# Kernel tuning notes

Hardware: AMD Instinct MI355X
Metric: run time of the kernel (lower is better)

Reference implementation:

```python
import jax, jax.numpy as jnp
import numpy as np

HEIGHT = 32
SIGMA = 2.0
NUM_NEGATIVE = 4096
N, C = 32, 512
L = HEIGHT * HEIGHT


def _grid_weight(height: int, sigma: float) -> jnp.ndarray:
    # distance_weights: pairwise Euclidean distance between grid points
    ii, jj = np.meshgrid(np.arange(height), np.arange(height), indexing='ij')
    coords = np.stack([ii.ravel(), jj.ravel()], axis=1).astype(np.float32)  # [L, 2]
    d2 = ((coords[:, None, :] - coords[None, :, :]) ** 2).sum(-1)  # squared dist [L, L]
    w = -(0.5 / sigma ** 2) * d2
    np.fill_diagonal(w, -np.inf)
    return jax.nn.softmax(jnp.asarray(w, dtype=jnp.float32), axis=1)


def setup_inputs() -> dict:
    key = jax.random.key(0)
    k1, k2 = jax.random.split(key)
    embedding = jax.random.normal(k1, (N, L, C), dtype=jnp.float32)
    weight = _grid_weight(HEIGHT, SIGMA)  # [L, L] softmax-normalized grid kernel
    neg_indices = jax.random.randint(k2, (NUM_NEGATIVE,), 0, N * L, dtype=jnp.int64)
    return {"embedding": embedding, "weight": weight, "neg_indices": neg_indices}


def reference(embedding, weight, neg_indices):
    n, l, c = embedding.shape
    # F.normalize(dim=-1), eps=1e-12
    norm = jnp.maximum(jnp.linalg.norm(embedding, axis=-1, keepdims=True), 1e-12)
    e = embedding / norm  # [N, L, C]
    # target = weight @ e  (broadcast over batch)
    target = jnp.einsum('kl,nlc->nkc', weight, e)  # [N, L, C]
    sim_pos = jnp.sum(e * target, axis=-1)  # [N, L]
    flat = e.reshape(-1, c)  # [N*L, C]
    negatives = flat[neg_indices]  # [M, C]
    sim_neg = jnp.einsum('nlc,mc->nlm', e, negatives)  # [N, L, M]
    logits = jnp.concatenate([sim_pos[..., None], sim_neg], axis=2).reshape(n * l, 1 + neg_indices.shape[0])
    # CrossEntropyLoss with target class 0, mean reduction
    loss = -jnp.mean(jax.nn.log_softmax(logits, axis=-1)[:, 0])
    return loss
```

## Files before the change

kernel.cpp:

```cpp
#include <hip/hip_runtime.h>
#include <hip/hip_bf16.h>
#include <stdint.h>

#define L_DIM 1024
#define C_DIM 512
#define CB4 256
#define N_BATCH 32
#define M_NEG 4096
#define NROWS (N_BATCH * L_DIM)

typedef float f32x4 __attribute__((ext_vector_type(4)));
typedef int i32x4 __attribute__((ext_vector_type(4)));
typedef int i32x8 __attribute__((ext_vector_type(8)));

#define E4_SCALE 32.0f
#define MX_SCALE 122
#define FMT_FP4 4

template <int GOFF>
__device__ __forceinline__ void gl_lds16(const uint8_t* g, uint8_t* l) {
  __builtin_amdgcn_global_load_lds(
      (const __attribute__((address_space(1))) void*)g,
      (__attribute__((address_space(3))) void*)l, 16, GOFF, 0);
}

__device__ __forceinline__ uint32_t fp4_enc(float x) {
  const uint32_t s = (__float_as_uint(x) >> 31) << 3;
  const float a = fabsf(x);
  uint32_t c;
  c = a < 0.25f ? 0u
    : a < 0.75f ? 1u
    : a < 1.25f ? 2u
    : a < 1.75f ? 3u
    : a < 2.5f  ? 4u
    : a < 3.5f  ? 5u
    : a < 5.0f  ? 6u : 7u;
  return s | c;
}

__device__ __forceinline__ i32x8 fp4_op(i32x4 d) {
  return __builtin_shufflevector(d, d, 0, 1, 2, 3, -1, -1, -1, -1);
}

__device__ __forceinline__ int swz(int row) { return (row >> 1) & 3; }

__global__ __launch_bounds__(256) void k_normalize(const float* __restrict__ emb,
                                                   uint8_t* __restrict__ out,
                                                   float* __restrict__ zerobuf,
                                                   float* __restrict__ loss_out) {
  if (blockIdx.x < 256) zerobuf[blockIdx.x * 256 + threadIdx.x] = 0.0f;
  if (blockIdx.x == 0 && threadIdx.x == 0) loss_out[0] = 0.0f;
  const int lane = threadIdx.x & 63;
  const int wave = threadIdx.x >> 6;
  const long row = (long)blockIdx.x * 4 + wave;
  const float4* src = (const float4*)(emb + row * C_DIM);
  float4 v0 = src[2 * lane];
  float4 v1 = src[2 * lane + 1];
  float ss = v0.x * v0.x + v0.y * v0.y + v0.z * v0.z + v0.w * v0.w +
             v1.x * v1.x + v1.y * v1.y + v1.z * v1.z + v1.w * v1.w;
#pragma unroll
  for (int off = 1; off < 64; off <<= 1) ss += __shfl_xor(ss, off, 64);
  const float s = E4_SCALE / fmaxf(sqrtf(ss), 1e-12f);
  uint32_t pk = fp4_enc(v0.x * s)        | (fp4_enc(v0.y * s) << 4) |
                (fp4_enc(v0.z * s) << 8) | (fp4_enc(v0.w * s) << 12) |
                (fp4_enc(v1.x * s) << 16)| (fp4_enc(v1.y * s) << 20) |
                (fp4_enc(v1.z * s) << 24)| (fp4_enc(v1.w * s) << 28);
  ((uint32_t*)(out + row * CB4))[lane] = pk;
}

__global__ __launch_bounds__(256, 4) void k_gemm_fused(
    const uint8_t* __restrict__ E4, const int* __restrict__ idx,
    const float* __restrict__ W, float* __restrict__ rowsum,
    float* __restrict__ simpos) {
  __shared__ __align__(16) unsigned char smem_raw[20480];
  uint8_t* sA = (uint8_t*)smem_raw;
  uint8_t* sB = sA + 128 * 64;

  const int tid = threadIdx.x;
  const int lane = tid & 63;
  const int wave = tid >> 6;
  const int wm = wave >> 1, wn = wave & 1;
  const int q = lane >> 4, c16 = lane & 15;

  const int bid = blockIdx.x;
  const bool is0 = bid >= 2048;
  long rowBase, colBase, n = 0;
  if (is0) {
    const int t = bid - 2048;
    const int xcd = t & 7, slot = t >> 3;
    rowBase = (long)(xcd * 32 + (slot & 31)) * 128;
    colBase = (long)(slot >> 5) * 128;
  } else {
    const int xcd = bid & 7, slot = bid >> 3;
    n = xcd * 4 + (slot & 3);
    const int inner = slot >> 2;
    rowBase = (long)(inner & 7) * 128;
    colBase = (long)(inner >> 3) * 128;
  }
  const long aBase = is0 ? rowBase : n * L_DIM + rowBase;

  const uint8_t* pA[2];
  const uint8_t* pB[2];
#pragma unroll
  for (int r = 0; r < 2; ++r) {
    const int c = r * 256 + tid;
    const int rw = c >> 2, cb = c & 3;
    pA[r] = E4 + (aBase + rw) * CB4 + (cb ^ swz(rw)) * 16;
    const long bRow = is0 ? (long)idx[colBase + rw] : n * L_DIM + colBase + rw;
    pB[r] = E4 + bRow * CB4 + (cb ^ swz(rw)) * 16;
  }

  int ldsB[4], ldsA[4];
#pragma unroll
  for (int j = 0; j < 4; ++j) {
    const int rowB = wn * 64 + j * 16 + c16;
    ldsB[j] = rowB * 64 + (q ^ swz(rowB)) * 16;
    const int rowA = wm * 64 + j * 16 + c16;
    ldsA[j] = rowA * 64 + (q ^ swz(rowA)) * 16;
  }

  f32x4 acc[4][4] = {};

  auto kstep = [&]() {
    __syncthreads();
    i32x8 bfr[4];
#pragma unroll
    for (int j = 0; j < 4; ++j)
      bfr[j] = fp4_op(*(const i32x4*)(sB + ldsB[j]));
#pragma unroll
    for (int i = 0; i < 4; ++i) {
      i32x8 af = fp4_op(*(const i32x4*)(sA + ldsA[i]));
#pragma unroll
      for (int j = 0; j < 4; ++j)
        acc[i][j] = __builtin_amdgcn_mfma_scale_f32_16x16x128_f8f6f4(
            af, bfr[j], acc[i][j], FMT_FP4, FMT_FP4,
            0, MX_SCALE, 0, MX_SCALE);
    }
    __syncthreads();
  };

  gl_lds16<0>(pA[0], sA + tid * 16);
  gl_lds16<0>(pA[1], sA + (256 + tid) * 16);
  gl_lds16<0>(pB[0], sB + tid * 16);
  gl_lds16<0>(pB[1], sB + (256 + tid) * 16);
  kstep();
  gl_lds16<64>(pA[0], sA + tid * 16);
  gl_lds16<64>(pA[1], sA + (256 + tid) * 16);
  gl_lds16<64>(pB[0], sB + tid * 16);
  gl_lds16<64>(pB[1], sB + (256 + tid) * 16);
  kstep();
  gl_lds16<128>(pA[0], sA + tid * 16);
  gl_lds16<128>(pA[1], sA + (256 + tid) * 16);
  gl_lds16<128>(pB[0], sB + tid * 16);
  gl_lds16<128>(pB[1], sB + (256 + tid) * 16);
  kstep();
  gl_lds16<192>(pA[0], sA + tid * 16);
  gl_lds16<192>(pA[1], sA + (256 + tid) * 16);
  gl_lds16<192>(pB[0], sB + tid * 16);
  gl_lds16<192>(pB[1], sB + (256 + tid) * 16);
  kstep();

  if (is0) {
    float* S = (float*)smem_raw;
#pragma unroll
    for (int i = 0; i < 4; ++i)
#pragma unroll
      for (int r = 0; r < 4; ++r) {
        const float s = __expf(acc[i][0][r]) + __expf(acc[i][1][r]) +
                        __expf(acc[i][2][r]) + __expf(acc[i][3][r]);
        S[wave * 1280 + (i * 16 + q * 4 + r) * 20 + c16] = s;
      }
    __syncthreads();
    if (tid < 128) {
      const int wm2 = tid >> 6, row64 = tid & 63;
      const float* p0 = (const float*)S + (wm2 * 2 + 0) * 1280 + row64 * 20;
      const float* p1 = (const float*)S + (wm2 * 2 + 1) * 1280 + row64 * 20;
      float4 t0 = ((const float4*)p0)[0], t1 = ((const float4*)p0)[1];
      float4 t2 = ((const float4*)p0)[2], t3 = ((const float4*)p0)[3];
      float4 u0 = ((const float4*)p1)[0], u1 = ((const float4*)p1)[1];
      float4 u2 = ((const float4*)p1)[2], u3 = ((const float4*)p1)[3];
      float v = t0.x + t0.y + t0.z + t0.w + t1.x + t1.y + t1.z + t1.w +
                t2.x + t2.y + t2.z + t2.w + t3.x + t3.y + t3.z + t3.w +
                u0.x + u0.y + u0.z + u0.w + u1.x + u1.y + u1.z + u1.w +
                u2.x + u2.y + u2.z + u2.w + u3.x + u3.y + u3.z + u3.w;
      atomicAdd(&rowsum[rowBase + tid], v);
    }
  } else {
    float* G = (float*)smem_raw;
#pragma unroll
    for (int p = 0; p < 4; ++p) {
      if (wm == (p >> 1)) {
#pragma unroll
        for (int ii = 0; ii < 2; ++ii) {
          const int i = (p & 1) * 2 + ii;
#pragma unroll
          for (int j = 0; j < 4; ++j)
#pragma unroll
            for (int r = 0; r < 4; ++r)
              G[(ii * 16 + q * 4 + r) * 132 + wn * 64 + j * 16 + c16] =
                  acc[i][j][r];
        }
      }
      __syncthreads();
      {
        const int rr = tid >> 3;
        const int chunk = tid & 7;
        const long krow = rowBase + p * 32 + rr;
        float v = 0.0f;
#pragma unroll
        for (int u = 0; u < 4; ++u) {
          const float4 g =
              *(const float4*)(G + rr * 132 + chunk * 16 + u * 4);
          const float4 w4 = *(const float4*)(W + krow * L_DIM + colBase +
                                             chunk * 16 + u * 4);
          v += g.x * w4.x + g.y * w4.y + g.z * w4.z + g.w * w4.w;
        }
        v += __shfl_xor(v, 1, 64);
        v += __shfl_xor(v, 2, 64);
        v += __shfl_xor(v, 4, 64);
        if (chunk == 0) atomicAdd(&simpos[n * L_DIM + krow], v);
      }
      __syncthreads();
    }
  }
}

__global__ __launch_bounds__(256) void k_finalize(const float* __restrict__ rowsum,
                                                  const float* __restrict__ simpos,
                                                  float* __restrict__ out) {
  const int gid = blockIdx.x * 256 + threadIdx.x;
  const float sp = simpos[gid];
  float v = __logf(rowsum[gid] + __expf(sp)) - sp;
#pragma unroll
  for (int off = 1; off < 64; off <<= 1) v += __shfl_xor(v, off, 64);
  __shared__ float ws[4];
  if ((threadIdx.x & 63) == 0) ws[threadIdx.x >> 6] = v;
  __syncthreads();
  if (threadIdx.x == 0)
    atomicAdd(out, (ws[0] + ws[1] + ws[2] + ws[3]) * (1.0f / (float)NROWS));
}

extern "C" void kernel_launch(void* const* d_in, const int* in_sizes, int n_in,
                              void* d_out, int out_size, void* d_ws, size_t ws_size,
                              hipStream_t stream) {
  const float* emb = (const float*)d_in[0];
  const float* weight = (const float*)d_in[1];
  const int* negidx = (const int*)d_in[2];
  float* out = (float*)d_out;
  char* ws = (char*)d_ws;

  uint8_t* E4 = (uint8_t*)ws;
  float* rowsum = (float*)(ws + 8388608);
  float* simpos = (float*)(ws + 8519680);

  k_normalize<<<NROWS / 4, 256, 0, stream>>>(emb, E4, rowsum, out);
  k_gemm_fused<<<10240, 256, 0, stream>>>(E4, negidx, weight, rowsum, simpos);
  k_finalize<<<NROWS / 256, 256, 0, stream>>>(rowsum, simpos, out);
}
```

Baseline: 165.0 us.

## Keep negative tile resident in LDS and stream embedding tiles per block

The negative-similarity GEMM blocks now load a 128-row negative tile (all K) into LDS once and loop over 8 embedding tiles of 128 rows. They accumulate exp sums per embedding row through shuffles and atomics rather than an LDS reduction. This cuts the grid from 10240 to 3072 blocks and removes repeated gathers of negative rows. The cost is doubled LDS (40KB) per block, which lowers occupancy, and less parallelism per block, with the exp-sum work serialized across the 8 tiles.

```diff
diff --git a/kernel.cpp b/kernel.cpp
--- a/kernel.cpp
+++ b/kernel.cpp
@@ -72,9 +72,7 @@
     const uint8_t* __restrict__ E4, const int* __restrict__ idx,
     const float* __restrict__ W, float* __restrict__ rowsum,
     float* __restrict__ simpos) {
-  __shared__ __align__(16) unsigned char smem_raw[20480];
-  uint8_t* sA = (uint8_t*)smem_raw;
-  uint8_t* sB = sA + 128 * 64;
+  __shared__ __align__(16) unsigned char smem_raw[40960];
 
   const int tid = threadIdx.x;
   const int lane = tid & 63;
@@ -83,109 +81,162 @@
   const int q = lane >> 4, c16 = lane & 15;
 
   const int bid = blockIdx.x;
-  const bool is0 = bid >= 2048;
-  long rowBase, colBase, n = 0;
-  if (is0) {
-    const int t = bid - 2048;
+
+  if (bid < 1024) {
+    uint8_t* sN = (uint8_t*)smem_raw;
+    uint8_t* sE = sN + 32768;
+    const int xcd = bid & 7, slot = bid >> 3;
+    const long negBase = (long)(slot & 31) * 128;
+    const long eBase0 = (long)(xcd * 4 + (slot >> 5)) * 1024;
+
+    const uint8_t* pN[2];
+#pragma unroll
+    for (int r = 0; r < 2; ++r) {
+      const int c = r * 256 + tid;
+      const int rw = c >> 2, cb = c & 3;
+      pN[r] = E4 + (long)idx[negBase + rw] * CB4 + (cb ^ swz(rw)) * 16;
+    }
+    gl_lds16<0>(pN[0], sN + tid * 16);
+    gl_lds16<0>(pN[1], sN + (256 + tid) * 16);
+    gl_lds16<64>(pN[0], sN + 8192 + tid * 16);
+    gl_lds16<64>(pN[1], sN + 8192 + (256 + tid) * 16);
+    gl_lds16<128>(pN[0], sN + 16384 + tid * 16);
+    gl_lds16<128>(pN[1], sN + 16384 + (256 + tid) * 16);
+    gl_lds16<192>(pN[0], sN + 24576 + tid * 16);
+    gl_lds16<192>(pN[1], sN + 24576 + (256 + tid) * 16);
+
+    const uint8_t* pE[2];
+#pragma unroll
+    for (int r = 0; r < 2; ++r) {
+      const int c = r * 256 + tid;
+      const int rw = c >> 2, cb = c & 3;
+      pE[r] = E4 + (eBase0 + rw) * CB4 + (cb ^ swz(rw)) * 16;
+    }
+
+    int ldsN[4], ldsE[4];
+#pragma unroll
+    for (int j = 0; j < 4; ++j) {
+      const int rowN = wm * 64 + j * 16 + c16;
+      ldsN[j] = rowN * 64 + (q ^ swz(rowN)) * 16;
+      const int rowE = wn * 64 + j * 16 + c16;
+      ldsE[j] = rowE * 64 + (q ^ swz(rowE)) * 16;
+    }
+
+    for (int et = 0; et < 8; ++et) {
+      f32x4 acc[4][4] = {};
+      auto kstep = [&](int ks) {
+        __syncthreads();
+        i32x8 efr[4];
+#pragma unroll
+        for (int j = 0; j < 4; ++j)
+          efr[j] = fp4_op(*(const i32x4*)(sE + ldsE[j]));
+#pragma unroll
+        for (int i = 0; i < 4; ++i) {
+          i32x8 nf = fp4_op(*(const i32x4*)(sN + ks * 8192 + ldsN[i]));
+#pragma unroll
+          for (int j = 0; j < 4; ++j)
+            acc[i][j] = __builtin_amdgcn_mfma_scale_f32_16x16x128_f8f6f4(
+                nf, efr[j], acc[i][j], FMT_FP4, FMT_FP4,
+                0, MX_SCALE, 0, MX_SCALE);
+        }
+        __syncthreads();
+      };
+      gl_lds16<0>(pE[0], sE + tid * 16);
+      gl_lds16<0>(pE[1], sE + (256 + tid) * 16);
+      kstep(0);
+      gl_lds16<64>(pE[0], sE + tid * 16);
+      gl_lds16<64>(pE[1], sE + (256 + tid) * 16);
+      kstep(1);
+      gl_lds16<128>(pE[0], sE + tid * 16);
+      gl_lds16<128>(pE[1], sE + (256 + tid) * 16);
+      kstep(2);
+      gl_lds16<192>(pE[0], sE + tid * 16);
+      gl_lds16<192>(pE[1], sE + (256 + tid) * 16);
+      kstep(3);
+      pE[0] += 32768;
+      pE[1] += 32768;
+
+      const long eCol = eBase0 + (long)et * 128 + wn * 64 + c16;
+#pragma unroll
+      for (int j = 0; j < 4; ++j) {
+        float s = 0.0f;
+#pragma unroll
+        for (int i = 0; i < 4; ++i)
+#pragma unroll
+          for (int r = 0; r < 4; ++r) s += __expf(acc[i][j][r]);
+        s += __shfl_xor(s, 16, 64);
+        s += __shfl_xor(s, 32, 64);
+        if (q == 0) atomicAdd(&rowsum[eCol + j * 16], s);
+      }
+    }
+  } else {
+    uint8_t* sA = (uint8_t*)smem_raw;
+    uint8_t* sB = sA + 8192;
+    const int t = bid - 1024;
     const int xcd = t & 7, slot = t >> 3;
-    rowBase = (long)(xcd * 32 + (slot & 31)) * 128;
-    colBase = (long)(slot >> 5) * 128;
-  } else {
-    const int xcd = bid & 7, slot = bid >> 3;
-    n = xcd * 4 + (slot & 3);
+    const long n = xcd * 4 + (slot & 3);
     const int inner = slot >> 2;
-    rowBase = (long)(inner & 7) * 128;
-    colBase = (long)(inner >> 3) * 128;
-  }
-  const long aBase = is0 ? rowBase : n * L_DIM + rowBase;
-
-  const uint8_t* pA[2];
-  const uint8_t* pB[2];
-#pragma unroll
-  for (int r = 0; r < 2; ++r) {
-    const int c = r * 256 + tid;
-    const int rw = c >> 2, cb = c & 3;
-    pA[r] = E4 + (aBase + rw) * CB4 + (cb ^ swz(rw)) * 16;
-    const long bRow = is0 ? (long)idx[colBase + rw] : n * L_DIM + colBase + rw;
-    pB[r] = E4 + bRow * CB4 + (cb ^ swz(rw)) * 16;
-  }
-
-  int ldsB[4], ldsA[4];
-#pragma unroll
-  for (int j = 0; j < 4; ++j) {
-    const int rowB = wn * 64 + j * 16 + c16;
-    ldsB[j] = rowB * 64 + (q ^ swz(rowB)) * 16;
-    const int rowA = wm * 64 + j * 16 + c16;
-    ldsA[j] = rowA * 64 + (q ^ swz(rowA)) * 16;
-  }
-
-  f32x4 acc[4][4] = {};
-
-  auto kstep = [&]() {
-    __syncthreads();
-    i32x8 bfr[4];
-#pragma unroll
-    for (int j = 0; j < 4; ++j)
-      bfr[j] = fp4_op(*(const i32x4*)(sB + ldsB[j]));
-#pragma unroll
-    for (int i = 0; i < 4; ++i) {
-      i32x8 af = fp4_op(*(const i32x4*)(sA + ldsA[i]));
+    const long rowBase = (long)(inner & 7) * 128;
+    const long colBase = (long)(inner >> 3) * 128;
+    const long aBase = n * L_DIM + rowBase;
+
+    const uint8_t* pA[2];
+    const uint8_t* pB[2];
+#pragma unroll
+    for (int r = 0; r < 2; ++r) {
+      const int c = r * 256 + tid;
+      const int rw = c >> 2, cb = c & 3;
+      pA[r] = E4 + (aBase + rw) * CB4 + (cb ^ swz(rw)) * 16;
+      pB[r] = E4 + (n * L_DIM + colBase + rw) * CB4 + (cb ^ swz(rw)) * 16;
+    }
+    int ldsB[4], ldsA[4];
+#pragma unroll
+    for (int j = 0; j < 4; ++j) {
+      const int rowB = wn * 64 + j * 16 + c16;
+      ldsB[j] = rowB * 64 + (q ^ swz(rowB)) * 16;
+      const int rowA = wm * 64 + j * 16 + c16;
+      ldsA[j] = rowA * 64 + (q ^ swz(rowA)) * 16;
+    }
+
+    f32x4 acc[4][4] = {};
+    auto kstep = [&]() {
+      __syncthreads();
+      i32x8 bfr[4];
 #pragma unroll
       for (int j = 0; j < 4; ++j)
-        acc[i][j] = __builtin_amdgcn_mfma_scale_f32_16x16x128_f8f6f4(
-            af, bfr[j], acc[i][j], FMT_FP4, FMT_FP4,
-            0, MX_SCALE, 0, MX_SCALE);
-    }
-    __syncthreads();
-  };
-
-  gl_lds16<0>(pA[0], sA + tid * 16);
-  gl_lds16<0>(pA[1], sA + (256 + tid) * 16);
-  gl_lds16<0>(pB[0], sB + tid * 16);
-  gl_lds16<0>(pB[1], sB + (256 + tid) * 16);
-  kstep();
-  gl_lds16<64>(pA[0], sA + tid * 16);
-  gl_lds16<64>(pA[1], sA + (256 + tid) * 16);
-  gl_lds16<64>(pB[0], sB + tid * 16);
-  gl_lds16<64>(pB[1], sB + (256 + tid) * 16);
-  kstep();
-  gl_lds16<128>(pA[0], sA + tid * 16);
-  gl_lds16<128>(pA[1], sA + (256 + tid) * 16);
-  gl_lds16<128>(pB[0], sB + tid * 16);
-  gl_lds16<128>(pB[1], sB + (256 + tid) * 16);
-  kstep();
-  gl_lds16<192>(pA[0], sA + tid * 16);
-  gl_lds16<192>(pA[1], sA + (256 + tid) * 16);
-  gl_lds16<192>(pB[0], sB + tid * 16);
-  gl_lds16<192>(pB[1], sB + (256 + tid) * 16);
-  kstep();
-
-  if (is0) {
-    float* S = (float*)smem_raw;
-#pragma unroll
-    for (int i = 0; i < 4; ++i)
-#pragma unroll
-      for (int r = 0; r < 4; ++r) {
-        const float s = __expf(acc[i][0][r]) + __expf(acc[i][1][r]) +
-                        __expf(acc[i][2][r]) + __expf(acc[i][3][r]);
-        S[wave * 1280 + (i * 16 + q * 4 + r) * 20 + c16] = s;
+        bfr[j] = fp4_op(*(const i32x4*)(sB + ldsB[j]));
+#pragma unroll
+      for (int i = 0; i < 4; ++i) {
+        i32x8 af = fp4_op(*(const i32x4*)(sA + ldsA[i]));
+#pragma unroll
+        for (int j = 0; j < 4; ++j)
+          acc[i][j] = __builtin_amdgcn_mfma_scale_f32_16x16x128_f8f6f4(
+              af, bfr[j], acc[i][j], FMT_FP4, FMT_FP4,
+              0, MX_SCALE, 0, MX_SCALE);
       }
-    __syncthreads();
-    if (tid < 128) {
-      const int wm2 = tid >> 6, row64 = tid & 63;
-      const float* p0 = (const float*)S + (wm2 * 2 + 0) * 1280 + row64 * 20;
-      const float* p1 = (const float*)S + (wm2 * 2 + 1) * 1280 + row64 * 20;
-      float4 t0 = ((const float4*)p0)[0], t1 = ((const float4*)p0)[1];
-      float4 t2 = ((const float4*)p0)[2], t3 = ((const float4*)p0)[3];
-      float4 u0 = ((const float4*)p1)[0], u1 = ((const float4*)p1)[1];
-      float4 u2 = ((const float4*)p1)[2], u3 = ((const float4*)p1)[3];
-      float v = t0.x + t0.y + t0.z + t0.w + t1.x + t1.y + t1.z + t1.w +
-                t2.x + t2.y + t2.z + t2.w + t3.x + t3.y + t3.z + t3.w +
-                u0.x + u0.y + u0.z + u0.w + u1.x + u1.y + u1.z + u1.w +
-                u2.x + u2.y + u2.z + u2.w + u3.x + u3.y + u3.z + u3.w;
-      atomicAdd(&rowsum[rowBase + tid], v);
-    }
-  } else {
+      __syncthreads();
+    };
+    gl_lds16<0>(pA[0], sA + tid * 16);
+    gl_lds16<0>(pA[1], sA + (256 + tid) * 16);
+    gl_lds16<0>(pB[0], sB + tid * 16);
+    gl_lds16<0>(pB[1], sB + (256 + tid) * 16);
+    kstep();
+    gl_lds16<64>(pA[0], sA + tid * 16);
+    gl_lds16<64>(pA[1], sA + (256 + tid) * 16);
+    gl_lds16<64>(pB[0], sB + tid * 16);
+    gl_lds16<64>(pB[1], sB + (256 + tid) * 16);
+    kstep();
+    gl_lds16<128>(pA[0], sA + tid * 16);
+    gl_lds16<128>(pA[1], sA + (256 + tid) * 16);
+    gl_lds16<128>(pB[0], sB + tid * 16);
+    gl_lds16<128>(pB[1], sB + (256 + tid) * 16);
+    kstep();
+    gl_lds16<192>(pA[0], sA + tid * 16);
+    gl_lds16<192>(pA[1], sA + (256 + tid) * 16);
+    gl_lds16<192>(pB[0], sB + tid * 16);
+    gl_lds16<192>(pB[1], sB + (256 + tid) * 16);
+    kstep();
+
     float* G = (float*)smem_raw;
 #pragma unroll
     for (int p = 0; p < 4; ++p) {
@@ -209,8 +260,7 @@
         float v = 0.0f;
 #pragma unroll
         for (int u = 0; u < 4; ++u) {
-          const float4 g =
-              *(const float4*)(G + rr * 132 + chunk * 16 + u * 4);
+          const float4 g = *(const float4*)(G + rr * 132 + chunk * 16 + u * 4);
           const float4 w4 = *(const float4*)(W + krow * L_DIM + colBase +
                                              chunk * 16 + u * 4);
           v += g.x * w4.x + g.y * w4.y + g.z * w4.z + g.w * w4.w;
@@ -254,6 +304,6 @@
   float* simpos = (float*)(ws + 8519680);
 
   k_normalize<<<NROWS / 4, 256, 0, stream>>>(emb, E4, rowsum, out);
-  k_gemm_fused<<<10240, 256, 0, stream>>>(E4, negidx, weight, rowsum, simpos);
+  k_gemm_fused<<<3072, 256, 0, stream>>>(E4, negidx, weight, rowsum, simpos);
   k_finalize<<<NROWS / 256, 256, 0, stream>>>(rowsum, simpos, out);
 }
```

New measurement: 190.3 us. 1.15x slower.
